# Optimization experiments

Measured on AMD Instinct MI355X. Metric: run time of the kernel, lower is better.

Reference implementation:

```python
import jax, jax.numpy as jnp
import numpy as np

INNER_DIM = 128
GRU_DIM = 256
HAN_DIM = 512  # hidden_size_HANLayer * num_heads_HANLayer = 64 * 8
B = 32
N = 8192


def setup_inputs() -> dict:
    key = jax.random.key(0)
    k1, k2, k3, k4, k5 = jax.random.split(key, 5)
    change_embeddings = jax.random.normal(k1, (B, N, GRU_DIM), dtype=jnp.float32)
    edges_embeddings = jax.random.normal(k2, (N, HAN_DIM), dtype=jnp.float32)
    mask = jax.random.randint(k3, (B, N), 0, 2) == 1
    # nn.Linear weights: [out_features, in_features], no bias
    Wq = jax.random.normal(k4, (INNER_DIM, GRU_DIM), dtype=jnp.float32) * (GRU_DIM ** -0.5)
    Wk = jax.random.normal(k5, (INNER_DIM, HAN_DIM), dtype=jnp.float32) * (HAN_DIM ** -0.5)
    return {"change_embeddings": change_embeddings, "edges_embeddings": edges_embeddings,
            "mask": mask, "Wq": Wq, "Wk": Wk}


def reference(change_embeddings, edges_embeddings, mask, Wq, Wk):
    # k: [n, inner]
    k = edges_embeddings @ Wk.T
    # q: [B, n, inner]  (per-batch projection of change embeddings)
    q = jnp.einsum('bnd,ed->bne', change_embeddings, Wq)
    # Original computes full [n,n] q@k^T per batch then takes diag; that is just
    # the row-wise dot product q[b,j] . k[j], computed directly here.
    sim = jnp.einsum('bne,ne->bn', q, k) * (INNER_DIM ** -0.5)  # [B, n]
    mask_sim = jnp.where(mask, sim, jnp.float32(-1e9))
    out = jax.nn.softmax(mask_sim, axis=0)  # softmax over the batch dim
    return out.T  # [n, B]
```

## Files before the change

kernel.cpp:

```cpp
#include <hip/hip_runtime.h>

#define NTOK 8192
#define BDIM 32
#define GRU  256
#define HAN  512
#define INNER 128
static constexpr float SCALE = 0.08838834764831845f;

template <bool B_T>
__global__ __launch_bounds__(512) void gemm_tile(const float* __restrict__ A,
                                                 const float* __restrict__ B,
                                                 float* __restrict__ C,
                                                 int M, int K, int J, float alpha) {
    __shared__ float As[32][68];
    __shared__ float Bs[32][68];

    const int t  = threadIdx.x;
    const int n0 = blockIdx.x * 64;
    const int j0 = blockIdx.y * 64;
    const int tn = t >> 5;
    const int tj = t & 31;

    const int r_l = t >> 3;
    const int kq  = t & 7;

    float acc[4][2];
#pragma unroll
    for (int i = 0; i < 4; ++i) { acc[i][0] = 0.0f; acc[i][1] = 0.0f; }

    for (int kc = 0; kc < K; kc += 32) {
        {
            const float4 a = *(const float4*)(A + (size_t)(n0 + r_l) * K + kc + kq * 4);
            As[kq * 4 + 0][r_l] = a.x;
            As[kq * 4 + 1][r_l] = a.y;
            As[kq * 4 + 2][r_l] = a.z;
            As[kq * 4 + 3][r_l] = a.w;
        }
        if (B_T) {
            const float4 b = *(const float4*)(B + (size_t)(j0 + r_l) * K + kc + kq * 4);
            Bs[kq * 4 + 0][r_l] = b.x;
            Bs[kq * 4 + 1][r_l] = b.y;
            Bs[kq * 4 + 2][r_l] = b.z;
            Bs[kq * 4 + 3][r_l] = b.w;
        } else {
            const int k_l = t >> 4;
            const int j4  = (t & 15) * 4;
            *(float4*)&Bs[k_l][j4] =
                *(const float4*)(B + (size_t)(kc + k_l) * J + j0 + j4);
        }
        __syncthreads();

#pragma unroll
        for (int kk = 0; kk < 32; ++kk) {
            const float4 a4 = *(const float4*)&As[kk][tn * 4];
            const float2 b2 = *(const float2*)&Bs[kk][tj * 2];
            acc[0][0] = fmaf(a4.x, b2.x, acc[0][0]);
            acc[0][1] = fmaf(a4.x, b2.y, acc[0][1]);
            acc[1][0] = fmaf(a4.y, b2.x, acc[1][0]);
            acc[1][1] = fmaf(a4.y, b2.y, acc[1][1]);
            acc[2][0] = fmaf(a4.z, b2.x, acc[2][0]);
            acc[2][1] = fmaf(a4.z, b2.y, acc[2][1]);
            acc[3][0] = fmaf(a4.w, b2.x, acc[3][0]);
            acc[3][1] = fmaf(a4.w, b2.y, acc[3][1]);
        }
        __syncthreads();
    }

#pragma unroll
    for (int i = 0; i < 4; ++i) {
        float2 o;
        o.x = acc[i][0] * alpha;
        o.y = acc[i][1] * alpha;
        *(float2*)(C + (size_t)(n0 + tn * 4 + i) * J + j0 + tj * 2) = o;
    }
}

__global__ __launch_bounds__(512) void cal_sim_main(const float* __restrict__ chg,
                                                    const void* __restrict__ maskp,
                                                    const float* __restrict__ w,
                                                    float* __restrict__ out) {
    __shared__ float sim[BDIM][17];
    __shared__ float mrow[16], srow[16];
    __shared__ int mask_is_int;

    const int t  = threadIdx.x;
    const int n0 = blockIdx.x * 16;

    if (t == 0) {
        const unsigned int* mi = (const unsigned int*)maskp;
        int ok = 1;
        for (int i = 0; i < 64; ++i) ok &= (mi[i] <= 1u);
        mask_is_int = ok;
    }

    const int wave = t >> 6;
    const int half = (t >> 5) & 1;
    const int dq   = t & 31;
    const int nloc = wave * 2 + half;
    const int n    = n0 + nloc;

    float4 wr0 = *(const float4*)(w + (size_t)n * GRU + dq * 8);
    float4 wr1 = *(const float4*)(w + (size_t)n * GRU + dq * 8 + 4);

    __syncthreads();
    const int misi = mask_is_int;
    const int* mi = (const int*)maskp;
    const unsigned char* mb = (const unsigned char*)maskp;

    for (int b = 0; b < BDIM; ++b) {
        const float* cp = chg + ((size_t)b * NTOK + n) * GRU + dq * 8;
        const float4 c0 = *(const float4*)(cp);
        const float4 c1 = *(const float4*)(cp + 4);
        float p;
        p = c0.x * wr0.x;
        p = fmaf(c0.y, wr0.y, p);
        p = fmaf(c0.z, wr0.z, p);
        p = fmaf(c0.w, wr0.w, p);
        p = fmaf(c1.x, wr1.x, p);
        p = fmaf(c1.y, wr1.y, p);
        p = fmaf(c1.z, wr1.z, p);
        p = fmaf(c1.w, wr1.w, p);
        p += __shfl_xor(p, 1, 64);
        p += __shfl_xor(p, 2, 64);
        p += __shfl_xor(p, 4, 64);
        p += __shfl_xor(p, 8, 64);
        p += __shfl_xor(p, 16, 64);
        if (dq == 0) {
            const size_t mofs = (size_t)b * NTOK + n;
            const int mval = misi ? mi[mofs] : (int)mb[mofs];
            sim[b][nloc] = mval ? p : -1e9f;
        }
    }
    __syncthreads();

    if (t < 16) {
        float m = sim[0][t];
        for (int b = 1; b < BDIM; ++b) m = fmaxf(m, sim[b][t]);
        float s = 0.0f;
        for (int b = 0; b < BDIM; ++b) s += __expf(sim[b][t] - m);
        mrow[t] = m;
        srow[t] = 1.0f / s;
    }
    __syncthreads();

    {
        const int b  = t & 31;
        const int nl = t >> 5;
        out[(size_t)n0 * BDIM + t] = __expf(sim[b][nl] - mrow[nl]) * srow[nl];
    }
}

extern "C" void kernel_launch(void* const* d_in, const int* in_sizes, int n_in,
                              void* d_out, int out_size, void* d_ws, size_t ws_size,
                              hipStream_t stream) {
    const float* chg   = (const float*)d_in[0];
    const float* edges = (const float*)d_in[1];
    const void*  mask  = d_in[2];
    const float* Wq    = (const float*)d_in[3];
    const float* Wk    = (const float*)d_in[4];
    float* out = (float*)d_out;

    float* kws = (float*)d_ws;
    float* wws = kws + (size_t)NTOK * INNER;

    gemm_tile<true><<<dim3(NTOK / 64, INNER / 64), 512, 0, stream>>>(
        edges, Wk, kws, NTOK, HAN, INNER, 1.0f);

    gemm_tile<false><<<dim3(NTOK / 64, GRU / 64), 512, 0, stream>>>(
        kws, Wq, wws, NTOK, INNER, GRU, SCALE);

    cal_sim_main<<<NTOK / 16, 512, 0, stream>>>(chg, mask, wws, out);
}
```

Baseline: 410.3 us.

## Precompute Wk^T·Wq product and fold scale, widen GEMM register tile

```diff
diff --git a/kernel.cpp b/kernel.cpp
--- a/kernel.cpp
+++ b/kernel.cpp
@@ -7,91 +7,104 @@
 #define INNER 128
 static constexpr float SCALE = 0.08838834764831845f;
 
-template <bool B_T>
-__global__ __launch_bounds__(512) void gemm_tile(const float* __restrict__ A,
+__global__ __launch_bounds__(256) void make_m(const float* __restrict__ Wk,
+                                              const float* __restrict__ Wq,
+                                              const void* __restrict__ maskp,
+                                              float* __restrict__ M,
+                                              int* __restrict__ flag) {
+    const int e = blockIdx.x;
+    const int j = threadIdx.x;
+    float acc = 0.0f;
+#pragma unroll 8
+    for (int i = 0; i < INNER; ++i)
+        acc = fmaf(Wk[(size_t)i * HAN + e], Wq[(size_t)i * GRU + j], acc);
+    M[(size_t)e * GRU + j] = SCALE * acc;
+
+    if (e == 0 && j < 64) {
+        const unsigned int* mi = (const unsigned int*)maskp;
+        const int ok = __all((int)(mi[j] <= 1u)) ? 1 : 0;
+        if (j == 0) *flag = ok;
+    }
+}
+
+__global__ __launch_bounds__(256) void gemm_tile(const float* __restrict__ A,
                                                  const float* __restrict__ B,
                                                  float* __restrict__ C,
-                                                 int M, int K, int J, float alpha) {
+                                                 int M, int K, int J) {
     __shared__ float As[32][68];
     __shared__ float Bs[32][68];
 
     const int t  = threadIdx.x;
     const int n0 = blockIdx.x * 64;
     const int j0 = blockIdx.y * 64;
-    const int tn = t >> 5;
-    const int tj = t & 31;
+    const int tn = t >> 4;
+    const int tj = t & 15;
 
-    const int r_l = t >> 3;
-    const int kq  = t & 7;
+    const int r_l = t >> 2;
+    const int kq  = t & 3;
+    const int k_l = t >> 4;
+    const int j4  = (t & 15) * 4;
 
-    float acc[4][2];
+    float acc[4][4];
 #pragma unroll
-    for (int i = 0; i < 4; ++i) { acc[i][0] = 0.0f; acc[i][1] = 0.0f; }
+    for (int i = 0; i < 4; ++i)
+#pragma unroll
+        for (int j = 0; j < 4; ++j) acc[i][j] = 0.0f;
 
     for (int kc = 0; kc < K; kc += 32) {
-        {
-            const float4 a = *(const float4*)(A + (size_t)(n0 + r_l) * K + kc + kq * 4);
-            As[kq * 4 + 0][r_l] = a.x;
-            As[kq * 4 + 1][r_l] = a.y;
-            As[kq * 4 + 2][r_l] = a.z;
-            As[kq * 4 + 3][r_l] = a.w;
+#pragma unroll
+        for (int h = 0; h < 2; ++h) {
+            const int kb = kq * 4 + h * 16;
+            const float4 a = *(const float4*)(A + (size_t)(n0 + r_l) * K + kc + kb);
+            As[kb + 0][r_l] = a.x;
+            As[kb + 1][r_l] = a.y;
+            As[kb + 2][r_l] = a.z;
+            As[kb + 3][r_l] = a.w;
         }
-        if (B_T) {
-            const float4 b = *(const float4*)(B + (size_t)(j0 + r_l) * K + kc + kq * 4);
-            Bs[kq * 4 + 0][r_l] = b.x;
-            Bs[kq * 4 + 1][r_l] = b.y;
-            Bs[kq * 4 + 2][r_l] = b.z;
-            Bs[kq * 4 + 3][r_l] = b.w;
-        } else {
-            const int k_l = t >> 4;
-            const int j4  = (t & 15) * 4;
-            *(float4*)&Bs[k_l][j4] =
-                *(const float4*)(B + (size_t)(kc + k_l) * J + j0 + j4);
+#pragma unroll
+        for (int h = 0; h < 2; ++h) {
+            const int kr = k_l + h * 16;
+            *(float4*)&Bs[kr][j4] =
+                *(const float4*)(B + (size_t)(kc + kr) * J + j0 + j4);
         }
         __syncthreads();
 
 #pragma unroll
         for (int kk = 0; kk < 32; ++kk) {
             const float4 a4 = *(const float4*)&As[kk][tn * 4];
-            const float2 b2 = *(const float2*)&Bs[kk][tj * 2];
-            acc[0][0] = fmaf(a4.x, b2.x, acc[0][0]);
-            acc[0][1] = fmaf(a4.x, b2.y, acc[0][1]);
-            acc[1][0] = fmaf(a4.y, b2.x, acc[1][0]);
-            acc[1][1] = fmaf(a4.y, b2.y, acc[1][1]);
-            acc[2][0] = fmaf(a4.z, b2.x, acc[2][0]);
-            acc[2][1] = fmaf(a4.z, b2.y, acc[2][1]);
-            acc[3][0] = fmaf(a4.w, b2.x, acc[3][0]);
-            acc[3][1] = fmaf(a4.w, b2.y, acc[3][1]);
+            const float4 b4 = *(const float4*)&Bs[kk][tj * 4];
+            const float av[4] = {a4.x, a4.y, a4.z, a4.w};
+            const float bv[4] = {b4.x, b4.y, b4.z, b4.w};
+#pragma unroll
+            for (int i = 0; i < 4; ++i)
+#pragma unroll
+                for (int j = 0; j < 4; ++j)
+                    acc[i][j] = fmaf(av[i], bv[j], acc[i][j]);
         }
         __syncthreads();
     }
 
 #pragma unroll
     for (int i = 0; i < 4; ++i) {
-        float2 o;
-        o.x = acc[i][0] * alpha;
-        o.y = acc[i][1] * alpha;
-        *(float2*)(C + (size_t)(n0 + tn * 4 + i) * J + j0 + tj * 2) = o;
+        float4 o;
+        o.x = acc[i][0];
+        o.y = acc[i][1];
+        o.z = acc[i][2];
+        o.w = acc[i][3];
+        *(float4*)(C + (size_t)(n0 + tn * 4 + i) * J + j0 + tj * 4) = o;
     }
 }
 
 __global__ __launch_bounds__(512) void cal_sim_main(const float* __restrict__ chg,
                                                     const void* __restrict__ maskp,
                                                     const float* __restrict__ w,
+                                                    const int* __restrict__ flag,
                                                     float* __restrict__ out) {
     __shared__ float sim[BDIM][17];
     __shared__ float mrow[16], srow[16];
-    __shared__ int mask_is_int;
 
     const int t  = threadIdx.x;
     const int n0 = blockIdx.x * 16;
-
-    if (t == 0) {
-        const unsigned int* mi = (const unsigned int*)maskp;
-        int ok = 1;
-        for (int i = 0; i < 64; ++i) ok &= (mi[i] <= 1u);
-        mask_is_int = ok;
-    }
 
     const int wave = t >> 6;
     const int half = (t >> 5) & 1;
@@ -99,14 +112,14 @@
     const int nloc = wave * 2 + half;
     const int n    = n0 + nloc;
 
-    float4 wr0 = *(const float4*)(w + (size_t)n * GRU + dq * 8);
-    float4 wr1 = *(const float4*)(w + (size_t)n * GRU + dq * 8 + 4);
+    const float4 wr0 = *(const float4*)(w + (size_t)n * GRU + dq * 8);
+    const float4 wr1 = *(const float4*)(w + (size_t)n * GRU + dq * 8 + 4);
 
-    __syncthreads();
-    const int misi = mask_is_int;
+    const int misi = *flag;
     const int* mi = (const int*)maskp;
     const unsigned char* mb = (const unsigned char*)maskp;
 
+#pragma unroll 8
     for (int b = 0; b < BDIM; ++b) {
         const float* cp = chg + ((size_t)b * NTOK + n) * GRU + dq * 8;
         const float4 c0 = *(const float4*)(cp);
@@ -160,14 +173,14 @@
     const float* Wk    = (const float*)d_in[4];
     float* out = (float*)d_out;
 
-    float* kws = (float*)d_ws;
-    float* wws = kws + (size_t)NTOK * INNER;
+    float* wws  = (float*)d_ws;
+    float* Mws  = wws + (size_t)NTOK * GRU;
+    int*   flag = (int*)(Mws + (size_t)HAN * GRU);
 
-    gemm_tile<true><<<dim3(NTOK / 64, INNER / 64), 512, 0, stream>>>(
-        edges, Wk, kws, NTOK, HAN, INNER, 1.0f);
+    make_m<<<HAN, 256, 0, stream>>>(Wk, Wq, mask, Mws, flag);
 
-    gemm_tile<false><<<dim3(NTOK / 64, GRU / 64), 512, 0, stream>>>(
-        kws, Wq, wws, NTOK, INNER, GRU, SCALE);
+    gemm_tile<<<dim3(NTOK / 64, GRU / 64), 256, 0, stream>>>(
+        edges, Mws, wws, NTOK, HAN, GRU);
 
-    cal_sim_main<<<NTOK / 16, 512, 0, stream>>>(chg, mask, wws, out);
+    cal_sim_main<<<NTOK / 16, 512, 0, stream>>>(chg, mask, wws, flag, out);
 }
```

New measurement: 408.1 us. No clear change (-0.5%).
